# Kernel optimization log

Measured on AMD Instinct MI355X. Metric: run time of the kernel, lower is better.

Reference implementation:

```python
import jax, jax.numpy as jnp
import numpy as np

N_WORD, N_TOPIC, N_DOC = 30000, 1000, 15000
D_WORD, D_TOPIC, D_OUT = 300, 300, 128
E = dict(ww=800000, wt=400000, wd=600000, td=300000, tt=150000)
SRC_N = dict(ww=N_WORD, wt=N_WORD, wd=N_WORD, td=N_TOPIC, tt=N_TOPIC)
DST_N = dict(ww=N_WORD, wt=N_TOPIC, wd=N_DOC, td=N_DOC, tt=N_TOPIC)


def setup_inputs() -> dict:
    key = jax.random.key(0)
    ks = iter(jax.random.split(key, 64))
    inp = {}
    inp["feat_word"] = jax.random.normal(next(ks), (N_WORD, D_WORD), jnp.float32)
    inp["feat_topic"] = jax.random.normal(next(ks), (N_TOPIC, D_TOPIC), jnp.float32)
    for et in ["ww", "wt", "wd", "td", "tt"]:
        inp[f"{et}_src"] = jax.random.randint(next(ks), (E[et],), 0, SRC_N[et], jnp.int32)
        inp[f"{et}_dst"] = jax.random.randint(next(ks), (E[et],), 0, DST_N[et], jnp.int32)
        inp[f"{et}_w"] = jax.random.uniform(next(ks), (E[et],), jnp.float32)
        din = D_WORD if et[0] == "w" else D_TOPIC
        inp[f"W_{et}"] = jax.random.normal(next(ks), (din, D_OUT), jnp.float32) / np.float32(np.sqrt(din))
        inp[f"b_{et}"] = jnp.zeros((D_OUT,), jnp.float32)
    return inp


def _mean_agg(Wh, src, dst, w, n_dst):
    # DGL fn.u_mul_e('Wh','weight','m') + fn.mean('m','h'): per-edge message
    # Wh[src] * w, mean-reduced per destination node (0 for isolated nodes).
    m = Wh[src] * w[:, None]                                   # [E, D_OUT]
    s = jax.ops.segment_sum(m, dst, num_segments=n_dst)        # [n_dst, D_OUT]
    c = jax.ops.segment_sum(jnp.ones_like(w), dst, num_segments=n_dst)
    return s / jnp.maximum(c, 1.0)[:, None]


def reference(feat_word, feat_topic,
              ww_src, ww_dst, ww_w, wt_src, wt_dst, wt_w,
              wd_src, wd_dst, wd_w, td_src, td_dst, td_w,
              tt_src, tt_dst, tt_w,
              W_ww, b_ww, W_wt, b_wt, W_wd, b_wd, W_td, b_td, W_tt, b_tt):
    # NOTE: the original forward's causal/noise branch is dead code --
    # `Wh = self.weight[etype](feat_dict[srctype])` overwrites it, so the
    # live math is a plain per-edge-type linear projection of source feats.
    Wh_ww = feat_word @ W_ww + b_ww
    Wh_wt = feat_word @ W_wt + b_wt
    Wh_wd = feat_word @ W_wd + b_wd
    Wh_td = feat_topic @ W_td + b_td
    Wh_tt = feat_topic @ W_tt + b_tt
    # multi_update_all(..., 'sum'): sum the per-etype means per dst node type.
    h_word = _mean_agg(Wh_ww, ww_src, ww_dst, ww_w, N_WORD)
    h_topic = (_mean_agg(Wh_wt, wt_src, wt_dst, wt_w, N_TOPIC)
               + _mean_agg(Wh_tt, tt_src, tt_dst, tt_w, N_TOPIC))
    h_doc = (_mean_agg(Wh_wd, wd_src, wd_dst, wd_w, N_DOC)
             + _mean_agg(Wh_td, td_src, td_dst, td_w, N_DOC))
    return (h_word, h_topic, h_doc)
```

## Files before the change

kernel.cpp:

```cpp
#include <hip/hip_runtime.h>

#define N_WORD 30000
#define N_TOPIC 1000
#define N_DOC 15000
#define DIN 300
#define KP 320
#define DOUT 128

#define E_WW 800000
#define E_WT 400000
#define E_WD 600000
#define E_TD 300000
#define E_TT 150000

#define CC_WW 0
#define CC_WT 30000
#define CC_WD 31000
#define CC_TD 46000
#define CC_TT 61000
#define NBINS 62000

#define CAP_WW 80
#define CAP_WT 544
#define CAP_WD 96
#define CAP_TD 56
#define CAP_TT 240
#define SB_WW 0
#define SB_WT (SB_WW + N_WORD * CAP_WW)
#define SB_WD (SB_WT + N_TOPIC * CAP_WT)
#define SB_TD (SB_WD + N_DOC * CAP_WD)
#define SB_TT (SB_TD + N_DOC * CAP_TD)
#define SLOT_TOTAL (SB_TT + N_TOPIC * CAP_TT)

#define CNT_BLOCKS 360
#define HIST_TOTAL 4168000

#define GW_ROW 469
#define GW_BLOCKS (GW_ROW * 3)
#define GT_ROW 16
#define GT_BLOCKS (GT_ROW * 2)
#define OFF_BLOCKS 243

#define GB_TOPIC 250
#define GB_DOC 3750
#define GB_WORD 7500

static inline int cdiv(int a, int b) { return (a + b - 1) / b; }

using half8  = __attribute__((ext_vector_type(8))) _Float16;
using half2v = __attribute__((ext_vector_type(2))) _Float16;
using f32x4  = __attribute__((ext_vector_type(4))) float;

struct SegP {
    const int* src[5];
    const int* dst[5];
    const float* w[5];
};

struct WPtrs {
    const float* W[5];
    const float* b[5];
};

__device__ __forceinline__ void decode_grp(
    int b, int& ti, int& hx, int& dlo, int& bins, int& hb,
    int& ch, int& ne, int& cap, int& sbase)
{
    if (b < 64)       { ti=0; hx=b;     dlo=0;     bins=15000; hb=0;       ch=12500; ne=E_WW; cap=CAP_WW; sbase=SB_WW; }
    else if (b < 128) { ti=0; hx=b-64;  dlo=15000; bins=15000; hb=960000;  ch=12500; ne=E_WW; cap=CAP_WW; sbase=SB_WW; }
    else if (b < 192) { ti=1; hx=b-128; dlo=0;     bins=1000;  hb=1920000; ch=6250;  ne=E_WT; cap=CAP_WT; sbase=SB_WT; }
    else if (b < 288) { ti=2; hx=b-192; dlo=0;     bins=15000; hb=1984000; ch=6250;  ne=E_WD; cap=CAP_WD; sbase=SB_WD; }
    else if (b < 336) { ti=3; hx=b-288; dlo=0;     bins=15000; hb=3424000; ch=6250;  ne=E_TD; cap=CAP_TD; sbase=SB_TD; }
    else              { ti=4; hx=b-336; dlo=0;     bins=1000;  hb=4144000; ch=6250;  ne=E_TT; cap=CAP_TT; sbase=SB_TT; }
}

__global__ __launch_bounds__(256) void prep_w(
    WPtrs WP, _Float16* __restrict__ Wt_word, _Float16* __restrict__ Wt_topic,
    float* __restrict__ bcat_word, float* __restrict__ bcat_topic)
{
    int id = blockIdx.x * 256 + threadIdx.x;
    const int total = (384 + 256) * KP;
    if (id >= total) return;
    int ng = id / KP;
    int k = id - ng * KP;
    int mat, n, lng;
    _Float16* Wt;
    float* bc;
    if (ng < 384) { lng = ng; mat = lng >> 7; Wt = Wt_word; bc = bcat_word; }
    else          { lng = ng - 384; mat = 3 + (lng >> 7); Wt = Wt_topic; bc = bcat_topic; }
    n = lng & 127;
    Wt[(size_t)lng * KP + k] =
        (k < DIN) ? (_Float16)WP.W[mat][(size_t)k * DOUT + n] : (_Float16)0.f;
    if (k == 0) bc[lng] = WP.b[mat][n];
}

__global__ __launch_bounds__(1024) void count_k(SegP S, int* __restrict__ hist)
{
    __shared__ int h[15000];
    int ti, hx, dlo, bins, hb, ch, ne, cap, sbase;
    decode_grp(blockIdx.x, ti, hx, dlo, bins, hb, ch, ne, cap, sbase);
    (void)cap; (void)sbase;
    for (int i = threadIdx.x; i < bins; i += 1024) h[i] = 0;
    __syncthreads();
    const int* __restrict__ dst = S.dst[ti];
    int lo = hx * ch;
    int hiE = lo + ch; if (hiE > ne) hiE = ne;
    for (int i = lo + (int)threadIdx.x; i < hiE; i += 1024) {
        int ld = dst[i] - dlo;
        if ((unsigned)ld < (unsigned)bins) atomicAdd(&h[ld], 1);
    }
    __syncthreads();
    int* __restrict__ out = hist + hb + hx * bins;
    for (int i = threadIdx.x; i < bins; i += 1024) out[i] = h[i];
}

__device__ __forceinline__ void gemm_direct(
    const float* __restrict__ A, int M,
    const _Float16* __restrict__ Wt, const float* __restrict__ bcat,
    _Float16* __restrict__ C, int Cstride, int rowBlk, int colBase)
{
    const int t = threadIdx.x;
    const int lane = t & 63;
    const int w = t >> 6;
    const int lm = lane & 15;
    const int lq = lane >> 4;
    const int rowBase = rowBlk * 64;
    const int arow = rowBase + w * 16 + lm;

    f32x4 acc[8];
#pragma unroll
    for (int j = 0; j < 8; ++j) acc[j] = f32x4{0.f, 0.f, 0.f, 0.f};

    for (int kb = 0; kb < KP; kb += 32) {
        const int k0 = kb + lq * 8;
        half8 af = half8{0, 0, 0, 0, 0, 0, 0, 0};
        if (arow < M) {
            const float* ap = A + (size_t)arow * DIN + k0;
            if (k0 + 8 <= DIN) {
                float4 f0 = *(const float4*)ap;
                float4 f1 = *(const float4*)(ap + 4);
                af = half8{(_Float16)f0.x, (_Float16)f0.y, (_Float16)f0.z,
                           (_Float16)f0.w, (_Float16)f1.x, (_Float16)f1.y,
                           (_Float16)f1.z, (_Float16)f1.w};
            } else if (k0 < DIN) {
#pragma unroll
                for (int j = 0; j < 8; ++j)
                    if (k0 + j < DIN) af[j] = (_Float16)ap[j];
            }
        }
#pragma unroll
        for (int jt = 0; jt < 8; ++jt) {
            int n = colBase + jt * 16 + lm;
            half8 bf = *(const half8*)&Wt[(size_t)n * KP + k0];
            acc[jt] = __builtin_amdgcn_mfma_f32_16x16x32_f16(af, bf, acc[jt], 0, 0, 0);
        }
    }

#pragma unroll
    for (int jt = 0; jt < 8; ++jt) {
        int col = colBase + jt * 16 + lm;
        float bias = bcat[col];
#pragma unroll
        for (int reg = 0; reg < 4; ++reg) {
            int gr = rowBase + w * 16 + lq * 4 + reg;
            if (gr < M)
                C[(size_t)gr * Cstride + col] = (_Float16)(acc[jt][reg] + bias);
        }
    }
}

__global__ __launch_bounds__(256, 5) void phaseB(
    int* __restrict__ hist, int* __restrict__ cnt,
    const float* __restrict__ Aw, const _Float16* __restrict__ Wtw,
    const float* __restrict__ bw, _Float16* __restrict__ Cw,
    const float* __restrict__ At, const _Float16* __restrict__ Wtt,
    const float* __restrict__ bt, _Float16* __restrict__ Ct)
{
    const int b = blockIdx.x;
    if (b < GW_BLOCKS) {
        int seg = b / GW_ROW;
        int rowBlk = b - seg * GW_ROW;
        gemm_direct(Aw, N_WORD, Wtw, bw, Cw, 384, rowBlk, seg * 128);
    } else if (b < GW_BLOCKS + GT_BLOCKS) {
        int g = b - GW_BLOCKS;
        int seg = g / GT_ROW;
        int rowBlk = g - seg * GT_ROW;
        gemm_direct(At, N_TOPIC, Wtt, bt, Ct, 256, rowBlk, seg * 128);
    } else {
        int g = (b - GW_BLOCKS - GT_BLOCKS) * 256 + (int)threadIdx.x;
        if (g < NBINS) {
            int lb, bins, hb, H;
            if (g < 15000)      { lb = g;         bins = 15000; hb = 0;       H = 64; }
            else if (g < 30000) { lb = g - 15000; bins = 15000; hb = 960000;  H = 64; }
            else if (g < 31000) { lb = g - 30000; bins = 1000;  hb = 1920000; H = 64; }
            else if (g < 46000) { lb = g - 31000; bins = 15000; hb = 1984000; H = 96; }
            else if (g < 61000) { lb = g - 46000; bins = 15000; hb = 3424000; H = 48; }
            else                { lb = g - 61000; bins = 1000;  hb = 4144000; H = 24; }
            int* __restrict__ p = hist + hb + lb;
            int run = 0;
            for (int h2 = 0; h2 < H; ++h2) {
                int v = p[(size_t)h2 * bins];
                p[(size_t)h2 * bins] = run;
                run += v;
            }
            cnt[g] = run;
        }
    }
}

__global__ __launch_bounds__(1024) void place_k(
    SegP S, const int* __restrict__ hist, unsigned int* __restrict__ slots)
{
    __shared__ int off[15000];
    int ti, hx, dlo, bins, hb, ch, ne, cap, sbase;
    decode_grp(blockIdx.x, ti, hx, dlo, bins, hb, ch, ne, cap, sbase);
    const int* __restrict__ po = hist + hb + hx * bins;
    for (int i = threadIdx.x; i < bins; i += 1024) off[i] = po[i];
    __syncthreads();
    const int* __restrict__ dst = S.dst[ti];
    const int* __restrict__ src = S.src[ti];
    const float* __restrict__ wp = S.w[ti];
    int lo = hx * ch;
    int hiE = lo + ch; if (hiE > ne) hiE = ne;
    for (int i = lo + (int)threadIdx.x; i < hiE; i += 1024) {
        int d = dst[i];
        int ld = d - dlo;
        if ((unsigned)ld < (unsigned)bins) {
            int pos = atomicAdd(&off[ld], 1);
            if (pos < cap) {
                unsigned short hw =
                    __builtin_bit_cast(unsigned short, (_Float16)wp[i]);
                slots[(size_t)sbase + (size_t)d * cap + pos] =
                    (unsigned int)src[i] | ((unsigned int)hw << 16);
            }
        }
    }
}

#define SV2(v, i) __builtin_shufflevector(v, v, i, i + 1)

__device__ __forceinline__ _Float16 wbits(unsigned int q)
{
    return __builtin_bit_cast(_Float16, (unsigned short)(q >> 16));
}

__device__ __forceinline__ void seg_mean16(
    const unsigned int* __restrict__ slots, int beg, int ce, int c,
    const _Float16* __restrict__ rowbase, int strideh, int ln, int sub,
    float a[8])
{
    half2v ac0 = half2v{0, 0}, ac1 = half2v{0, 0};
    half2v ac2 = half2v{0, 0}, ac3 = half2v{0, 0};
    int e = 0;
    for (; e + 16 <= ce; e += 16) {
        unsigned int q0 = slots[beg + e + 0 + sub];
        unsigned int q1 = slots[beg + e + 4 + sub];
        unsigned int q2 = slots[beg + e + 8 + sub];
        unsigned int q3 = slots[beg + e + 12 + sub];
        half8 v0 = *(const half8*)(rowbase + (size_t)(q0 & 0xFFFFu) * strideh + ln * 8);
        half8 v1 = *(const half8*)(rowbase + (size_t)(q1 & 0xFFFFu) * strideh + ln * 8);
        half8 v2 = *(const half8*)(rowbase + (size_t)(q2 & 0xFFFFu) * strideh + ln * 8);
        half8 v3 = *(const half8*)(rowbase + (size_t)(q3 & 0xFFFFu) * strideh + ln * 8);
        _Float16 h0 = wbits(q0), h1 = wbits(q1), h2 = wbits(q2), h3 = wbits(q3);
        half2v w0 = half2v{h0, h0}, w1 = half2v{h1, h1};
        half2v w2 = half2v{h2, h2}, w3 = half2v{h3, h3};
        ac0 += SV2(v0, 0) * w0 + SV2(v1, 0) * w1 + SV2(v2, 0) * w2 + SV2(v3, 0) * w3;
        ac1 += SV2(v0, 2) * w0 + SV2(v1, 2) * w1 + SV2(v2, 2) * w2 + SV2(v3, 2) * w3;
        ac2 += SV2(v0, 4) * w0 + SV2(v1, 4) * w1 + SV2(v2, 4) * w2 + SV2(v3, 4) * w3;
        ac3 += SV2(v0, 6) * w0 + SV2(v1, 6) * w1 + SV2(v2, 6) * w2 + SV2(v3, 6) * w3;
    }
    for (int e2 = e + sub; e2 < ce; e2 += 4) {
        unsigned int q = slots[beg + e2];
        half8 v = *(const half8*)(rowbase + (size_t)(q & 0xFFFFu) * strideh + ln * 8);
        _Float16 h = wbits(q);
        half2v wp = half2v{h, h};
        ac0 += SV2(v, 0) * wp;
        ac1 += SV2(v, 2) * wp;
        ac2 += SV2(v, 4) * wp;
        ac3 += SV2(v, 6) * wp;
    }
    a[0] = (float)ac0.x; a[1] = (float)ac0.y;
    a[2] = (float)ac1.x; a[3] = (float)ac1.y;
    a[4] = (float)ac2.x; a[5] = (float)ac2.y;
    a[6] = (float)ac3.x; a[7] = (float)ac3.y;
#pragma unroll
    for (int j = 0; j < 8; ++j) {
        a[j] += __shfl_down(a[j], 16);
        a[j] += __shfl_down(a[j], 32);
    }
    float inv = 1.0f / (float)(c > 1 ? c : 1);
#pragma unroll
    for (int j = 0; j < 8; ++j) a[j] *= inv;
}

__global__ __launch_bounds__(256) void gather_all(
    const unsigned int* __restrict__ slots, const int* __restrict__ cnt,
    const _Float16* __restrict__ Wh_word, const _Float16* __restrict__ Wh_topic,
    float* __restrict__ out_word, float* __restrict__ out_topic,
    float* __restrict__ out_doc)
{
    const int b = blockIdx.x;
    const int t = threadIdx.x;
    const int lane = t & 63;
    const int wv = t >> 6;
    const int sub = lane >> 4;
    const int ln = lane & 15;

    float a[8];
    float* outp;
    int node;

    if (b < GB_TOPIC) {
        node = b * 4 + wv;
        int c1 = cnt[CC_WT + node];
        int ce1 = c1 < CAP_WT ? c1 : CAP_WT;
        seg_mean16(slots, SB_WT + node * CAP_WT, ce1, c1, Wh_word + 128, 384, ln, sub, a);
        int c2 = cnt[CC_TT + node];
        int ce2 = c2 < CAP_TT ? c2 : CAP_TT;
        float a2[8];
        seg_mean16(slots, SB_TT + node * CAP_TT, ce2, c2, Wh_topic + 128, 256, ln, sub, a2);
#pragma unroll
        for (int j = 0; j < 8; ++j) a[j] += a2[j];
        outp = out_topic;
    } else if (b < GB_TOPIC + GB_DOC) {
        node = (b - GB_TOPIC) * 4 + wv;
        int c1 = cnt[CC_WD + node];
        int ce1 = c1 < CAP_WD ? c1 : CAP_WD;
        seg_mean16(slots, SB_WD + node * CAP_WD, ce1, c1, Wh_word + 256, 384, ln, sub, a);
        int c2 = cnt[CC_TD + node];
        int ce2 = c2 < CAP_TD ? c2 : CAP_TD;
        float a2[8];
        seg_mean16(slots, SB_TD + node * CAP_TD, ce2, c2, Wh_topic, 256, ln, sub, a2);
#pragma unroll
        for (int j = 0; j < 8; ++j) a[j] += a2[j];
        outp = out_doc;
    } else {
        node = (b - GB_TOPIC - GB_DOC) * 4 + wv;
        int c = cnt[CC_WW + node];
        int ce = c < CAP_WW ? c : CAP_WW;
        seg_mean16(slots, SB_WW + node * CAP_WW, ce, c, Wh_word, 384, ln, sub, a);
        outp = out_word;
    }

    if (sub == 0) {
        float4* o = (float4*)outp + (size_t)node * 32 + ln * 2;
        o[0] = make_float4(a[0], a[1], a[2], a[3]);
        o[1] = make_float4(a[4], a[5], a[6], a[7]);
    }
}

extern "C" void kernel_launch(void* const* d_in, const int* in_sizes, int n_in,
                              void* d_out, int out_size, void* d_ws, size_t ws_size,
                              hipStream_t stream)
{
    const float* feat_word  = (const float*)d_in[0];
    const float* feat_topic = (const float*)d_in[1];

    const int*   ww_src = (const int*)d_in[2];
    const int*   ww_dst = (const int*)d_in[3];
    const float* ww_w   = (const float*)d_in[4];
    const float* W_ww   = (const float*)d_in[5];
    const float* b_ww   = (const float*)d_in[6];

    const int*   wt_src = (const int*)d_in[7];
    const int*   wt_dst = (const int*)d_in[8];
    const float* wt_w   = (const float*)d_in[9];
    const float* W_wt   = (const float*)d_in[10];
    const float* b_wt   = (const float*)d_in[11];

    const int*   wd_src = (const int*)d_in[12];
    const int*   wd_dst = (const int*)d_in[13];
    const float* wd_w   = (const float*)d_in[14];
    const float* W_wd   = (const float*)d_in[15];
    const float* b_wd   = (const float*)d_in[16];

    const int*   td_src = (const int*)d_in[17];
    const int*   td_dst = (const int*)d_in[18];
    const float* td_w   = (const float*)d_in[19];
    const float* W_td   = (const float*)d_in[20];
    const float* b_td   = (const float*)d_in[21];

    const int*   tt_src = (const int*)d_in[22];
    const int*   tt_dst = (const int*)d_in[23];
    const float* tt_w   = (const float*)d_in[24];
    const float* W_tt   = (const float*)d_in[25];
    const float* b_tt   = (const float*)d_in[26];

    char* wsb = (char*)d_ws;
    size_t off = 0;
    _Float16* Wh_word  = (_Float16*)(wsb + off); off += (size_t)N_WORD * 384 * 2;
    _Float16* Wh_topic = (_Float16*)(wsb + off); off += (size_t)N_TOPIC * 256 * 2;
    _Float16* Wt_word  = (_Float16*)(wsb + off); off += (size_t)384 * KP * 2;
    _Float16* Wt_topic = (_Float16*)(wsb + off); off += (size_t)256 * KP * 2;
    float* bcat_word   = (float*)(wsb + off);    off += 384 * 4;
    float* bcat_topic  = (float*)(wsb + off);    off += 256 * 4;
    unsigned int* slots = (unsigned int*)(wsb + off); off += (size_t)SLOT_TOTAL * 4;
    int* cnt_all       = (int*)(wsb + off);      off += (size_t)NBINS * 4;
    int* hist          = (int*)(wsb + off);      off += (size_t)HIST_TOTAL * 4;

    float* out_word  = (float*)d_out;
    float* out_topic = out_word + (size_t)N_WORD * DOUT;
    float* out_doc   = out_topic + (size_t)N_TOPIC * DOUT;

    SegP S;
    S.src[0] = ww_src; S.dst[0] = ww_dst; S.w[0] = ww_w;
    S.src[1] = wt_src; S.dst[1] = wt_dst; S.w[1] = wt_w;
    S.src[2] = wd_src; S.dst[2] = wd_dst; S.w[2] = wd_w;
    S.src[3] = td_src; S.dst[3] = td_dst; S.w[3] = td_w;
    S.src[4] = tt_src; S.dst[4] = tt_dst; S.w[4] = tt_w;

    WPtrs WP;
    WP.W[0] = W_ww; WP.W[1] = W_wt; WP.W[2] = W_wd; WP.W[3] = W_td; WP.W[4] = W_tt;
    WP.b[0] = b_ww; WP.b[1] = b_wt; WP.b[2] = b_wd; WP.b[3] = b_td; WP.b[4] = b_tt;

    prep_w<<<cdiv((384 + 256) * KP, 256), 256, 0, stream>>>(
        WP, Wt_word, Wt_topic, bcat_word, bcat_topic);
    count_k<<<CNT_BLOCKS, 1024, 0, stream>>>(S, hist);
    phaseB<<<GW_BLOCKS + GT_BLOCKS + OFF_BLOCKS, 256, 0, stream>>>(
        hist, cnt_all,
        feat_word, Wt_word, bcat_word, Wh_word,
        feat_topic, Wt_topic, bcat_topic, Wh_topic);
    place_k<<<CNT_BLOCKS, 1024, 0, stream>>>(S, hist, slots);
    gather_all<<<GB_TOPIC + GB_DOC + GB_WORD, 256, 0, stream>>>(
        slots, cnt_all, Wh_word, Wh_topic, out_word, out_topic, out_doc);

    (void)in_sizes; (void)n_in; (void)ws_size;
}
```

Measured before the change: 354.6 us.

## Fuse weight prep into count kernel and compute all GEMM columns per block

Merges the weight-transpose prep kernel into the histogram count kernel, removing one launch. The GEMM now has each block compute all 384 (word) or 256 (topic) output columns for its 64 rows, so the fp32 A rows are read and converted once instead of once per 128-column segment. The prefix-scan blocks are reordered to run first, with a per-type tile decode and batched loads of 8 histogram entries. The larger accumulator arrays (24 MFMA tiles) raise register pressure, which is why the occupancy hint drops from 5 to 4, and there are fewer, heavier GEMM blocks.

```diff
diff --git a/kernel.cpp b/kernel.cpp
--- a/kernel.cpp
+++ b/kernel.cpp
@@ -33,19 +33,16 @@
 #define SLOT_TOTAL (SB_TT + N_TOPIC * CAP_TT)
 
 #define CNT_BLOCKS 360
+#define PREP_BLOCKS 200
 #define HIST_TOTAL 4168000
 
-#define GW_ROW 469
-#define GW_BLOCKS (GW_ROW * 3)
-#define GT_ROW 16
-#define GT_BLOCKS (GT_ROW * 2)
-#define OFF_BLOCKS 243
+#define PFX_BLOCKS 244
+#define GW_BLOCKS 469
+#define GT_BLOCKS 16
 
 #define GB_TOPIC 250
 #define GB_DOC 3750
 #define GB_WORD 7500
-
-static inline int cdiv(int a, int b) { return (a + b - 1) / b; }
 
 using half8  = __attribute__((ext_vector_type(8))) _Float16;
 using half2v = __attribute__((ext_vector_type(2))) _Float16;
@@ -74,50 +71,62 @@
     else              { ti=4; hx=b-336; dlo=0;     bins=1000;  hb=4144000; ch=6250;  ne=E_TT; cap=CAP_TT; sbase=SB_TT; }
 }
 
-__global__ __launch_bounds__(256) void prep_w(
+__device__ __forceinline__ void decode_pfx(
+    int b, int& hb, int& bins, int& H, int& cb, int& tile)
+{
+    if (b < 59)       { hb=0;       bins=15000; H=64; cb=0;     tile=b; }
+    else if (b < 118) { hb=960000;  bins=15000; H=64; cb=15000; tile=b-59; }
+    else if (b < 122) { hb=1920000; bins=1000;  H=64; cb=30000; tile=b-118; }
+    else if (b < 181) { hb=1984000; bins=15000; H=96; cb=31000; tile=b-122; }
+    else if (b < 240) { hb=3424000; bins=15000; H=48; cb=46000; tile=b-181; }
+    else              { hb=4144000; bins=1000;  H=24; cb=61000; tile=b-240; }
+}
+
+__global__ __launch_bounds__(1024) void prep_count(
+    SegP S, int* __restrict__ hist,
     WPtrs WP, _Float16* __restrict__ Wt_word, _Float16* __restrict__ Wt_topic,
     float* __restrict__ bcat_word, float* __restrict__ bcat_topic)
 {
-    int id = blockIdx.x * 256 + threadIdx.x;
-    const int total = (384 + 256) * KP;
-    if (id >= total) return;
-    int ng = id / KP;
-    int k = id - ng * KP;
-    int mat, n, lng;
-    _Float16* Wt;
-    float* bc;
-    if (ng < 384) { lng = ng; mat = lng >> 7; Wt = Wt_word; bc = bcat_word; }
-    else          { lng = ng - 384; mat = 3 + (lng >> 7); Wt = Wt_topic; bc = bcat_topic; }
-    n = lng & 127;
-    Wt[(size_t)lng * KP + k] =
-        (k < DIN) ? (_Float16)WP.W[mat][(size_t)k * DOUT + n] : (_Float16)0.f;
-    if (k == 0) bc[lng] = WP.b[mat][n];
-}
-
-__global__ __launch_bounds__(1024) void count_k(SegP S, int* __restrict__ hist)
-{
     __shared__ int h[15000];
-    int ti, hx, dlo, bins, hb, ch, ne, cap, sbase;
-    decode_grp(blockIdx.x, ti, hx, dlo, bins, hb, ch, ne, cap, sbase);
-    (void)cap; (void)sbase;
-    for (int i = threadIdx.x; i < bins; i += 1024) h[i] = 0;
-    __syncthreads();
-    const int* __restrict__ dst = S.dst[ti];
-    int lo = hx * ch;
-    int hiE = lo + ch; if (hiE > ne) hiE = ne;
-    for (int i = lo + (int)threadIdx.x; i < hiE; i += 1024) {
-        int ld = dst[i] - dlo;
-        if ((unsigned)ld < (unsigned)bins) atomicAdd(&h[ld], 1);
-    }
-    __syncthreads();
-    int* __restrict__ out = hist + hb + hx * bins;
-    for (int i = threadIdx.x; i < bins; i += 1024) out[i] = h[i];
-}
-
+    if (blockIdx.x < CNT_BLOCKS) {
+        int ti, hx, dlo, bins, hb, ch, ne, cap, sbase;
+        decode_grp(blockIdx.x, ti, hx, dlo, bins, hb, ch, ne, cap, sbase);
+        (void)cap; (void)sbase;
+        for (int i = threadIdx.x; i < bins; i += 1024) h[i] = 0;
+        __syncthreads();
+        const int* __restrict__ dst = S.dst[ti];
+        int lo = hx * ch;
+        int hiE = lo + ch; if (hiE > ne) hiE = ne;
+        for (int i = lo + (int)threadIdx.x; i < hiE; i += 1024) {
+            int ld = dst[i] - dlo;
+            if ((unsigned)ld < (unsigned)bins) atomicAdd(&h[ld], 1);
+        }
+        __syncthreads();
+        int* __restrict__ out = hist + hb + hx * bins;
+        for (int i = threadIdx.x; i < bins; i += 1024) out[i] = h[i];
+    } else {
+        int id = (blockIdx.x - CNT_BLOCKS) * 1024 + threadIdx.x;
+        const int total = (384 + 256) * KP;
+        if (id >= total) return;
+        int ng = id / KP;
+        int k = id - ng * KP;
+        int mat, n, lng;
+        _Float16* Wt;
+        float* bc;
+        if (ng < 384) { lng = ng; mat = lng >> 7; Wt = Wt_word; bc = bcat_word; }
+        else          { lng = ng - 384; mat = 3 + (lng >> 7); Wt = Wt_topic; bc = bcat_topic; }
+        n = lng & 127;
+        Wt[(size_t)lng * KP + k] =
+            (k < DIN) ? (_Float16)WP.W[mat][(size_t)k * DOUT + n] : (_Float16)0.f;
+        if (k == 0) bc[lng] = WP.b[mat][n];
+    }
+}
+
+template <int NJ>
 __device__ __forceinline__ void gemm_direct(
     const float* __restrict__ A, int M,
     const _Float16* __restrict__ Wt, const float* __restrict__ bcat,
-    _Float16* __restrict__ C, int Cstride, int rowBlk, int colBase)
+    _Float16* __restrict__ C, int Cstride, int rowBlk)
 {
     const int t = threadIdx.x;
     const int lane = t & 63;
@@ -127,9 +136,9 @@
     const int rowBase = rowBlk * 64;
     const int arow = rowBase + w * 16 + lm;
 
-    f32x4 acc[8];
-#pragma unroll
-    for (int j = 0; j < 8; ++j) acc[j] = f32x4{0.f, 0.f, 0.f, 0.f};
+    f32x4 acc[NJ];
+#pragma unroll
+    for (int j = 0; j < NJ; ++j) acc[j] = f32x4{0.f, 0.f, 0.f, 0.f};
 
     for (int kb = 0; kb < KP; kb += 32) {
         const int k0 = kb + lq * 8;
@@ -149,16 +158,16 @@
             }
         }
 #pragma unroll
-        for (int jt = 0; jt < 8; ++jt) {
-            int n = colBase + jt * 16 + lm;
+        for (int jt = 0; jt < NJ; ++jt) {
+            int n = jt * 16 + lm;
             half8 bf = *(const half8*)&Wt[(size_t)n * KP + k0];
             acc[jt] = __builtin_amdgcn_mfma_f32_16x16x32_f16(af, bf, acc[jt], 0, 0, 0);
         }
     }
 
 #pragma unroll
-    for (int jt = 0; jt < 8; ++jt) {
-        int col = colBase + jt * 16 + lm;
+    for (int jt = 0; jt < NJ; ++jt) {
+        int col = jt * 16 + lm;
         float bias = bcat[col];
 #pragma unroll
         for (int reg = 0; reg < 4; ++reg) {
@@ -169,7 +178,7 @@
     }
 }
 
-__global__ __launch_bounds__(256, 5) void phaseB(
+__global__ __launch_bounds__(256, 4) void phaseB(
     int* __restrict__ hist, int* __restrict__ cnt,
     const float* __restrict__ Aw, const _Float16* __restrict__ Wtw,
     const float* __restrict__ bw, _Float16* __restrict__ Cw,
@@ -177,34 +186,29 @@
     const float* __restrict__ bt, _Float16* __restrict__ Ct)
 {
     const int b = blockIdx.x;
-    if (b < GW_BLOCKS) {
-        int seg = b / GW_ROW;
-        int rowBlk = b - seg * GW_ROW;
-        gemm_direct(Aw, N_WORD, Wtw, bw, Cw, 384, rowBlk, seg * 128);
-    } else if (b < GW_BLOCKS + GT_BLOCKS) {
-        int g = b - GW_BLOCKS;
-        int seg = g / GT_ROW;
-        int rowBlk = g - seg * GT_ROW;
-        gemm_direct(At, N_TOPIC, Wtt, bt, Ct, 256, rowBlk, seg * 128);
+    if (b < PFX_BLOCKS) {
+        int hb, bins, H, cb, tile;
+        decode_pfx(b, hb, bins, H, cb, tile);
+        int g = tile * 256 + (int)threadIdx.x;
+        if (g < bins) {
+            int* __restrict__ p = hist + hb + g;
+            int run = 0;
+            for (int h0 = 0; h0 < H; h0 += 8) {
+                int v[8];
+#pragma unroll
+                for (int j = 0; j < 8; ++j) v[j] = p[(size_t)(h0 + j) * bins];
+#pragma unroll
+                for (int j = 0; j < 8; ++j) {
+                    p[(size_t)(h0 + j) * bins] = run;
+                    run += v[j];
+                }
+            }
+            cnt[cb + g] = run;
+        }
+    } else if (b < PFX_BLOCKS + GW_BLOCKS) {
+        gemm_direct<24>(Aw, N_WORD, Wtw, bw, Cw, 384, b - PFX_BLOCKS);
     } else {
-        int g = (b - GW_BLOCKS - GT_BLOCKS) * 256 + (int)threadIdx.x;
-        if (g < NBINS) {
-            int lb, bins, hb, H;
-            if (g < 15000)      { lb = g;         bins = 15000; hb = 0;       H = 64; }
-            else if (g < 30000) { lb = g - 15000; bins = 15000; hb = 960000;  H = 64; }
-            else if (g < 31000) { lb = g - 30000; bins = 1000;  hb = 1920000; H = 64; }
-            else if (g < 46000) { lb = g - 31000; bins = 15000; hb = 1984000; H = 96; }
-            else if (g < 61000) { lb = g - 46000; bins = 15000; hb = 3424000; H = 48; }
-            else                { lb = g - 61000; bins = 1000;  hb = 4144000; H = 24; }
-            int* __restrict__ p = hist + hb + lb;
-            int run = 0;
-            for (int h2 = 0; h2 < H; ++h2) {
-                int v = p[(size_t)h2 * bins];
-                p[(size_t)h2 * bins] = run;
-                run += v;
-            }
-            cnt[g] = run;
-        }
+        gemm_direct<16>(At, N_TOPIC, Wtt, bt, Ct, 256, b - PFX_BLOCKS - GW_BLOCKS);
     }
 }
 
@@ -413,10 +417,9 @@
     WP.W[0] = W_ww; WP.W[1] = W_wt; WP.W[2] = W_wd; WP.W[3] = W_td; WP.W[4] = W_tt;
     WP.b[0] = b_ww; WP.b[1] = b_wt; WP.b[2] = b_wd; WP.b[3] = b_td; WP.b[4] = b_tt;
 
-    prep_w<<<cdiv((384 + 256) * KP, 256), 256, 0, stream>>>(
-        WP, Wt_word, Wt_topic, bcat_word, bcat_topic);
-    count_k<<<CNT_BLOCKS, 1024, 0, stream>>>(S, hist);
-    phaseB<<<GW_BLOCKS + GT_BLOCKS + OFF_BLOCKS, 256, 0, stream>>>(
+    prep_count<<<CNT_BLOCKS + PREP_BLOCKS, 1024, 0, stream>>>(
+        S, hist, WP, Wt_word, Wt_topic, bcat_word, bcat_topic);
+    phaseB<<<PFX_BLOCKS + GW_BLOCKS + GT_BLOCKS, 256, 0, stream>>>(
         hist, cnt_all,
         feat_word, Wt_word, bcat_word, Wh_word,
         feat_topic, Wt_topic, bcat_topic, Wh_topic);
```

After: 325.4 us. 8.2% less time.
